# Kernel optimization log

Measured on AMD Instinct MI355X. Metric: run time of the kernel, lower is better.

Reference implementation:

```python
import jax, jax.numpy as jnp
import numpy as np
from jax import lax

B, T, D = 16, 4096, 512
L_OUT = 512          # fixed target length per batch row -> static max_label_len
THRESHOLD = 1.0
SMOOTH_FACTOR = 1.0
NOISE_THRESHOLD = 0.0


def setup_inputs() -> dict:
    key = jax.random.key(0)
    k1, k2, k3, k4 = jax.random.split(key, 4)
    hidden = jax.random.normal(k1, (B, T, D), dtype=jnp.float32)
    mask = jnp.ones((B, 1, T), dtype=jnp.float32)
    target_label_length = jnp.full((B, 1), float(L_OUT), dtype=jnp.float32)
    conv_w = jax.random.normal(k2, (D, D, 3), dtype=jnp.float32) * (1.0 / np.sqrt(3 * D))
    conv_b = jax.random.normal(k3, (D,), dtype=jnp.float32) * 0.02
    out_w = jax.random.normal(k4, (1, D), dtype=jnp.float32) * (1.0 / np.sqrt(D))
    out_b = jnp.zeros((1,), dtype=jnp.float32)
    return {"hidden": hidden, "mask": mask, "target_label_length": target_label_length,
            "conv_w": conv_w, "conv_b": conv_b, "out_w": out_w, "out_b": out_b}


def _cif(hidden, alphas, threshold, max_label_len):
    # hidden: [B,T,D], alphas: [B,T]
    b, t, d = hidden.shape

    def step(carry, xs):
        integrate, frame = carry          # [B], [B,D]
        alpha, h_t = xs                   # [B], [B,D]
        dist_completion = 1.0 - integrate
        integrate = integrate + alpha
        fires_t = integrate               # recorded BEFORE subtracting 1
        fire = integrate >= threshold
        integrate = jnp.where(fire, integrate - 1.0, integrate)
        cur = jnp.where(fire, dist_completion, alpha)
        remainds = alpha - cur
        frame = frame + cur[:, None] * h_t
        frames_t = frame                  # recorded BEFORE reset
        frame = jnp.where(fire[:, None], remainds[:, None] * h_t, frame)
        return (integrate, frame), (fires_t, frames_t)

    init = (jnp.zeros((b,), hidden.dtype), jnp.zeros((b, d), hidden.dtype))
    xs = (jnp.swapaxes(alphas, 0, 1), jnp.swapaxes(hidden, 0, 1))
    _, (fires, frames) = lax.scan(step, init, xs)
    fires = jnp.swapaxes(fires, 0, 1)     # [B,T]
    frames = jnp.swapaxes(frames, 0, 1)   # [B,T,D]

    # ragged gather of fired frames, padded to static max_label_len
    fire_mask = fires >= threshold                                  # [B,T]
    slot = jnp.cumsum(fire_mask.astype(jnp.int32), axis=1) - 1      # output slot per fire
    safe_slot = jnp.where(fire_mask, jnp.clip(slot, 0, max_label_len), max_label_len)
    out = jnp.zeros((b, max_label_len + 1, d), hidden.dtype)
    out = out.at[jnp.arange(b)[:, None], safe_slot].add(frames)     # non-fires -> dump row
    return out[:, :max_label_len, :], fires


def reference(hidden, mask, target_label_length, conv_w, conv_b, out_w, out_b):
    # conv over time: pad (l_order, r_order)=(1,1), kernel 3, relu
    x = jnp.swapaxes(hidden, 1, 2)                                  # [B,D,T]
    x = jnp.pad(x, ((0, 0), (0, 0), (1, 1)))
    y = lax.conv_general_dilated(x, conv_w, (1,), 'VALID',
                                 dimension_numbers=('NCH', 'OIH', 'NCH'))
    y = jax.nn.relu(y + conv_b[None, :, None])
    y = jnp.swapaxes(y, 1, 2)                                       # [B,T,D]
    a = y @ out_w.T + out_b                                         # [B,T,1]
    alphas = jax.nn.sigmoid(a)
    alphas = jax.nn.relu(alphas * SMOOTH_FACTOR - NOISE_THRESHOLD)
    alphas = alphas * jnp.swapaxes(mask, 1, 2)                      # [B,T,1]
    alphas = alphas[..., 0]                                         # [B,T]
    token_num = alphas.sum(-1)                                      # pre-scale sum (returned)
    target_length = target_label_length[:, 0]
    alphas = alphas * (target_length / token_num)[:, None]
    acoustic_embeds, cif_peak = _cif(hidden, alphas, THRESHOLD, L_OUT)
    return acoustic_embeds, token_num, alphas, cif_peak
```

## Files before the change

kernel.cpp:

```cpp
#include <hip/hip_runtime.h>
#include <math.h>

#define BB 16
#define TT 4096
#define DD 512
#define LOUT 512

typedef __attribute__((ext_vector_type(8))) _Float16 half8;
typedef __attribute__((ext_vector_type(4))) float floatx4;


__global__ void prep(const float* __restrict__ hidden,
                     const float* __restrict__ conv_w,
                     _Float16* __restrict__ A_hi,
                     _Float16* __restrict__ A_lo,
                     _Float16* __restrict__ B_hi,
                     _Float16* __restrict__ B_lo,
                     float* __restrict__ a_pre,
                     _Float16* __restrict__ zp) {
    int idx = blockIdx.x * 256 + threadIdx.x;
    const float4* src = (const float4*)(hidden + 8 * (size_t)idx);
    float4 v0 = src[0], v1 = src[1];
    float x[8] = {v0.x, v0.y, v0.z, v0.w, v1.x, v1.y, v1.z, v1.w};
    _Float16 hi[8], lo[8];
    #pragma unroll
    for (int j = 0; j < 8; j++) {
        hi[j] = (_Float16)x[j];
        lo[j] = (_Float16)(x[j] - (float)hi[j]);
    }
    *(half8*)(A_hi + 8 * (size_t)idx) = *(half8*)hi;
    *(half8*)(A_lo + 8 * (size_t)idx) = *(half8*)lo;

    if (idx < 786432) {
        int tap = idx / 262144;
        int rem = idx - tap * 262144;
        int c = rem >> 9;
        int i = rem & 511;
        float v = conv_w[(c * 512 + i) * 3 + tap];
        _Float16 h = (_Float16)v;
        B_hi[idx] = h;
        B_lo[idx] = (_Float16)(v - (float)h);
    }
    if (idx < 65536) a_pre[idx] = 0.f;
    if (idx < 512)   zp[idx] = (_Float16)0.f;
}

#define GLL16(g, l) __builtin_amdgcn_global_load_lds( \
    (const __attribute__((address_space(1))) void*)(g), \
    (__attribute__((address_space(3))) void*)(l), 16, 0, 0)

__launch_bounds__(256, 2)
__global__ void mfma_gemm(const char* __restrict__ wsb,
                          const float* __restrict__ conv_b,
                          const float* __restrict__ out_w,
                          float* __restrict__ a_pre) {
    __shared__ __align__(128) char lds[59392];

    const int tid  = threadIdx.x;
    const int w    = tid >> 6;
    const int lane = tid & 63;

    const int bid = blockIdx.x;
    const int swz = (bid & 7) * 256 + (bid >> 3);
    const int nt  = swz & 7;
    const int mt  = swz >> 3;
    const int b   = mt >> 4;
    const int t0  = (mt & 15) << 8;
    const int c0  = nt << 6;

    const int srow = lane >> 2;
    const int schk = lane & 3;

    int sgoff[15], sloff[15];
    #pragma unroll
    for (int j = 0; j < 15; j++) {
        const int g = w + 4 * j;
        int so = 137953344, lo = 0;
        if (g < 58) {
            if (g < 34) {
                const int dt = (g >= 17);
                const int u  = dt ? g - 17 : g;
                const int r  = 16 * u + srow;
                const int t  = t0 - 1 + r;
                const int sw = (schk ^ ((r >> 1) & 3)) << 4;
                so = (t >= 0 && t < TT) ? (dt ? 67108864 : 0)
                                          + (b * TT + t) * 1024 + sw
                                        : 137953344 + sw;
                lo = dt * 17408 + u * 1024;
            } else {
                const int h  = g - 34;
                const int dt = h / 12;
                const int rm = h % 12;
                const int tp = rm >> 2;
                const int u  = rm & 3;
                const int r  = 16 * u + srow;
                const int sw = (schk ^ ((r >> 1) & 3)) << 4;
                so = (dt ? 135790592 : 134217728) + tp * 524288
                     + (c0 + r) * 1024 + sw;
                lo = 34816 + dt * 12288 + tp * 4096 + u * 1024;
            }
        }
        sgoff[j] = so;
        sloff[j] = lo;
    }

    int aoff[12], boff[4];
    #pragma unroll
    for (int tap = 0; tap < 3; tap++)
        #pragma unroll
        for (int i = 0; i < 4; i++) {
            const int ra = 64 * w + 16 * i + (lane & 15) + tap;
            aoff[tap * 4 + i] = ra * 64
                + (((lane >> 4) ^ ((ra >> 1) & 3)) << 4);
        }
    #pragma unroll
    for (int i = 0; i < 4; i++) {
        const int rb = 16 * i + (lane & 15);
        boff[i] = rb * 64 + (((lane >> 4) ^ ((rb >> 1) & 3)) << 4);
    }

    floatx4 acc[4][4];
    #pragma unroll
    for (int mi = 0; mi < 4; mi++)
        #pragma unroll
        for (int ni = 0; ni < 4; ni++)
            acc[mi][ni] = (floatx4)(0.f);

    float u_n[4], cb_n[4];
    #pragma unroll
    for (int ni = 0; ni < 4; ni++) {
        int n = c0 + 16 * ni + (lane & 15);
        u_n[ni]  = out_w[n];
        cb_n[ni] = conv_b[n];
    }

    for (int kc = 0; kc < 16; kc++) {
        const int kb = kc << 6;

        #pragma unroll
        for (int j = 0; j < 15; j++)
            if (w + 4 * j < 58)
                GLL16(wsb + (size_t)(sgoff[j] + kb), lds + sloff[j]);
        __syncthreads();

        #pragma unroll
        for (int tap = 0; tap < 3; tap++) {
            half8 ah[4], al[4], bh[4], bl[4];
            #pragma unroll
            for (int i = 0; i < 4; i++) {
                ah[i] = *(const half8*)(lds + aoff[tap * 4 + i]);
                al[i] = *(const half8*)(lds + 17408 + aoff[tap * 4 + i]);
                bh[i] = *(const half8*)(lds + 34816 + tap * 4096 + boff[i]);
                bl[i] = *(const half8*)(lds + 47104 + tap * 4096 + boff[i]);
            }
            #pragma unroll
            for (int mi = 0; mi < 4; mi++)
                #pragma unroll
                for (int ni = 0; ni < 4; ni++)
                    acc[mi][ni] = __builtin_amdgcn_mfma_f32_16x16x32_f16(
                        ah[mi], bh[ni], acc[mi][ni], 0, 0, 0);
            #pragma unroll
            for (int mi = 0; mi < 4; mi++)
                #pragma unroll
                for (int ni = 0; ni < 4; ni++)
                    acc[mi][ni] = __builtin_amdgcn_mfma_f32_16x16x32_f16(
                        al[mi], bh[ni], acc[mi][ni], 0, 0, 0);
            #pragma unroll
            for (int mi = 0; mi < 4; mi++)
                #pragma unroll
                for (int ni = 0; ni < 4; ni++)
                    acc[mi][ni] = __builtin_amdgcn_mfma_f32_16x16x32_f16(
                        ah[mi], bl[ni], acc[mi][ni], 0, 0, 0);
        }
        __syncthreads();
    }

    float s[4][4];
    #pragma unroll
    for (int mi = 0; mi < 4; mi++)
        #pragma unroll
        for (int rg = 0; rg < 4; rg++) {
            float t = 0.f;
            #pragma unroll
            for (int ni = 0; ni < 4; ni++) {
                float y = acc[mi][ni][rg] + cb_n[ni];
                y = y > 0.f ? y : 0.f;
                t = fmaf(y, u_n[ni], t);
            }
            s[mi][rg] = t;
        }
    #pragma unroll
    for (int mi = 0; mi < 4; mi++)
        #pragma unroll
        for (int rg = 0; rg < 4; rg++) {
            #pragma unroll
            for (int off = 1; off < 16; off <<= 1)
                s[mi][rg] += __shfl_xor(s[mi][rg], off);
        }
    if ((lane & 15) == 0) {
        const int q = lane >> 4;
        #pragma unroll
        for (int mi = 0; mi < 4; mi++)
            #pragma unroll
            for (int rg = 0; rg < 4; rg++) {
                int m = 64 * w + 16 * mi + 4 * q + rg;
                atomicAdd(&a_pre[b * TT + t0 + m], s[mi][rg]);
            }
    }
}

__global__ void cif_scan(const float* __restrict__ a_pre,
                         const float* __restrict__ mask,
                         const float* __restrict__ tll,
                         const float* __restrict__ out_bias,
                         float* __restrict__ out_tn,
                         float* __restrict__ out_alphas,
                         float* __restrict__ out_peak,
                         float* __restrict__ w_main,
                         int* __restrict__ fire_pos,
                         int* __restrict__ Fcount) {
    __shared__ float alpha_s[TT];
    __shared__ float wm_s[TT];
    __shared__ float fires_s[TT];
    __shared__ int   fp_s[1024];
    __shared__ double red[256];
    __shared__ float ratio_s;
    __shared__ int   F_sh;

    const int b = blockIdx.x;
    const int tid = threadIdx.x;
    const float ob = out_bias[0];

    double lsum = 0.0;
    for (int t = tid; t < TT; t += 256) {
        float a = a_pre[b * TT + t] + ob;
        float e = expf(-fabsf(a));
        float sg = (a >= 0.f) ? (1.f / (1.f + e)) : (e / (1.f + e));
        float af = sg;
        af = af > 0.f ? af : 0.f;
        af = af * mask[b * TT + t];
        alpha_s[t] = af;
        lsum += (double)af;
    }
    red[tid] = lsum;
    __syncthreads();
    for (int off = 128; off > 0; off >>= 1) {
        if (tid < off) red[tid] += red[tid + off];
        __syncthreads();
    }
    if (tid == 0) {
        float tn = (float)red[0];
        out_tn[b] = tn;
        ratio_s = tll[b] / tn;
    }
    __syncthreads();
    const float ratio = ratio_s;

    const int t0c = tid * 16;
    float av[16];
    double csum = 0.0;
    #pragma unroll
    for (int j = 0; j < 16; j++) {
        float a = alpha_s[t0c + j] * ratio;
        av[j] = a;
        csum += (double)a;
    }
    #pragma unroll
    for (int j = 0; j < 16; j++)
        alpha_s[t0c + j] = av[j];
    red[tid] = csum;
    __syncthreads();

    #pragma unroll
    for (int off = 1; off < 256; off <<= 1) {
        double v = (tid >= off) ? red[tid - off] : 0.0;
        __syncthreads();
        red[tid] += v;
        __syncthreads();
    }
    const double base = red[tid] - csum;

    double P = base;
    int Fp = (int)P;
    #pragma unroll
    for (int j = 0; j < 16; j++) {
        const float a = av[j];
        const double Pp = P;
        P += (double)a;
        const int F = (int)P;
        fires_s[t0c + j] = (float)(P - (double)Fp);
        const bool fire = F > Fp;
        wm_s[t0c + j] = fire ? (float)((double)F - Pp) : a;
        if (fire && Fp < 1024) fp_s[Fp] = t0c + j;
        Fp = F;
    }
    if (tid == 255) {
        F_sh = (Fp > 1024) ? 1024 : Fp;
        Fcount[b] = F_sh;
    }
    __syncthreads();

    for (int t = tid; t < TT; t += 256) {
        out_alphas[b * TT + t] = alpha_s[t];
        out_peak[b * TT + t]   = fires_s[t];
        w_main[b * TT + t]     = wm_s[t];
    }
    const int F = F_sh;
    for (int s = tid; s < F; s += 256)
        fire_pos[b * 1024 + s] = fp_s[s];
}

__global__ void cif_scatter(const float* __restrict__ hidden,
                            const float* __restrict__ alphas,
                            const float* __restrict__ w_main,
                            const int* __restrict__ fire_pos,
                            const int* __restrict__ Fcount,
                            float* __restrict__ out_emb) {
    const int s = blockIdx.x;
    const int b = blockIdx.y;
    const int tid = threadIdx.x;
    const int F = Fcount[b];

    float4 acc = make_float4(0.f, 0.f, 0.f, 0.f);
    if (s < F) {
        const int t_hi = fire_pos[b * 1024 + s];
        const int t_lo = (s > 0) ? fire_pos[b * 1024 + s - 1] : 0;
        for (int t = t_lo; t <= t_hi; t++) {
            float w;
            if (s > 0 && t == t_lo)
                w = alphas[b * TT + t] - w_main[b * TT + t];
            else
                w = w_main[b * TT + t];
            const float4 h = *(const float4*)(hidden + ((size_t)(b * TT + t)) * DD + 4 * tid);
            acc.x = fmaf(w, h.x, acc.x);
            acc.y = fmaf(w, h.y, acc.y);
            acc.z = fmaf(w, h.z, acc.z);
            acc.w = fmaf(w, h.w, acc.w);
        }
    }
    *(float4*)(out_emb + ((size_t)(b * LOUT + s)) * DD + 4 * tid) = acc;
}

extern "C" void kernel_launch(void* const* d_in, const int* in_sizes, int n_in,
                              void* d_out, int out_size, void* d_ws, size_t ws_size,
                              hipStream_t stream) {
    const float* hidden  = (const float*)d_in[0];
    const float* mask    = (const float*)d_in[1];
    const float* tll     = (const float*)d_in[2];
    const float* conv_w  = (const float*)d_in[3];
    const float* conv_b  = (const float*)d_in[4];
    const float* out_w   = (const float*)d_in[5];
    const float* out_b   = (const float*)d_in[6];

    float* out        = (float*)d_out;
    float* out_emb    = out;
    float* out_tn     = out + 4194304;
    float* out_alphas = out + 4194320;
    float* out_peak   = out + 4259856;

    char* ws = (char*)d_ws;
    _Float16* A_hi   = (_Float16*)(ws);
    _Float16* A_lo   = (_Float16*)(ws + 67108864);
    _Float16* B_hi   = (_Float16*)(ws + 134217728);
    _Float16* B_lo   = (_Float16*)(ws + 135790592);
    float* a_pre     = (float*)(ws + 137363456);
    float* w_main    = (float*)(ws + 137625600);
    int*   fire_pos  = (int*)(ws + 137887744);
    int*   Fcount    = (int*)(ws + 137953280);
    _Float16* zpage  = (_Float16*)(ws + 137953344);

    prep<<<16384, 256, 0, stream>>>(hidden, conv_w, A_hi, A_lo, B_hi, B_lo,
                                    a_pre, zpage);
    mfma_gemm<<<2048, 256, 0, stream>>>(ws, conv_b, out_w, a_pre);
    cif_scan<<<16, 256, 0, stream>>>(a_pre, mask, tll, out_b,
                                     out_tn, out_alphas, out_peak,
                                     w_main, fire_pos, Fcount);
    cif_scatter<<<dim3(512, 16), 128, 0, stream>>>(hidden, out_alphas, w_main,
                                                   fire_pos, Fcount, out_emb);
}
```

Baseline: 509.9 us.

## Double-buffer LDS staging in MFMA conv GEMM to overlap loads with compute

The GEMM's K loop now uses two LDS buffers, so the async global-to-LDS loads for the next K chunk are issued while MFMAs run on the current one, with one barrier per half-step. LDS use doubles to about 116 KB through dynamic shared memory, and launch bounds drop from 2 to 1 block per CU. This trades occupancy, and with it the latency hiding that a second resident block gave, for explicit in-block overlap of memory and compute.

```diff
diff --git a/kernel.cpp b/kernel.cpp
--- a/kernel.cpp
+++ b/kernel.cpp
@@ -49,12 +49,54 @@
     (const __attribute__((address_space(1))) void*)(g), \
     (__attribute__((address_space(3))) void*)(l), 16, 0, 0)
 
-__launch_bounds__(256, 2)
+
+#define STAGE(KBX, WROFF)                                                    \
+  do {                                                                       \
+    _Pragma("unroll")                                                        \
+    for (int j_ = 0; j_ < 15; j_++)                                          \
+      if (w + 4 * j_ < 58)                                                   \
+        GLL16(wsb + (size_t)(sgoff[j_] + (KBX)), lds + (WROFF) + sloff[j_]); \
+  } while (0)
+
+#define COMPUTE(KB, RD)                                                      \
+  do {                                                                       \
+    _Pragma("unroll")                                                        \
+    for (int tap = 0; tap < 3; tap++) {                                      \
+      half8 ah[4], al[4], bh[4], bl[4];                                      \
+      _Pragma("unroll")                                                      \
+      for (int i = 0; i < 4; i++) {                                          \
+        ah[i] = *(const half8*)(lds + (RD) + aoff[tap * 4 + i]);             \
+        al[i] = *(const half8*)(lds + (RD) + 17408 + aoff[tap * 4 + i]);     \
+        bh[i] = *(const half8*)(lds + (RD) + 34816 + tap * 4096 + boff[i]);  \
+        bl[i] = *(const half8*)(lds + (RD) + 47104 + tap * 4096 + boff[i]);  \
+      }                                                                      \
+      _Pragma("unroll")                                                      \
+      for (int mi = 0; mi < 4; mi++)                                         \
+        _Pragma("unroll")                                                    \
+        for (int ni = 0; ni < 4; ni++)                                       \
+          acc[mi][ni] = __builtin_amdgcn_mfma_f32_16x16x32_f16(              \
+              ah[mi], bh[ni], acc[mi][ni], 0, 0, 0);                         \
+      _Pragma("unroll")                                                      \
+      for (int mi = 0; mi < 4; mi++)                                         \
+        _Pragma("unroll")                                                    \
+        for (int ni = 0; ni < 4; ni++)                                       \
+          acc[mi][ni] = __builtin_amdgcn_mfma_f32_16x16x32_f16(              \
+              al[mi], bh[ni], acc[mi][ni], 0, 0, 0);                         \
+      _Pragma("unroll")                                                      \
+      for (int mi = 0; mi < 4; mi++)                                         \
+        _Pragma("unroll")                                                    \
+        for (int ni = 0; ni < 4; ni++)                                       \
+          acc[mi][ni] = __builtin_amdgcn_mfma_f32_16x16x32_f16(              \
+              ah[mi], bl[ni], acc[mi][ni], 0, 0, 0);                         \
+    }                                                                        \
+  } while (0)
+
+__launch_bounds__(256, 1)
 __global__ void mfma_gemm(const char* __restrict__ wsb,
                           const float* __restrict__ conv_b,
                           const float* __restrict__ out_w,
                           float* __restrict__ a_pre) {
-    __shared__ __align__(128) char lds[59392];
+    extern __shared__ __align__(128) char lds[];
 
     const int tid  = threadIdx.x;
     const int w    = tid >> 6;
@@ -134,44 +176,16 @@
         cb_n[ni] = conv_b[n];
     }
 
-    for (int kc = 0; kc < 16; kc++) {
-        const int kb = kc << 6;
-
-        #pragma unroll
-        for (int j = 0; j < 15; j++)
-            if (w + 4 * j < 58)
-                GLL16(wsb + (size_t)(sgoff[j] + kb), lds + sloff[j]);
+    STAGE(0, 0);
+    __syncthreads();
+
+    for (int kp = 0; kp < 8; kp++) {
+        const int KB = kp << 7;
+        STAGE(KB + 64, 59392);
+        COMPUTE(KB, 0);
         __syncthreads();
-
-        #pragma unroll
-        for (int tap = 0; tap < 3; tap++) {
-            half8 ah[4], al[4], bh[4], bl[4];
-            #pragma unroll
-            for (int i = 0; i < 4; i++) {
-                ah[i] = *(const half8*)(lds + aoff[tap * 4 + i]);
-                al[i] = *(const half8*)(lds + 17408 + aoff[tap * 4 + i]);
-                bh[i] = *(const half8*)(lds + 34816 + tap * 4096 + boff[i]);
-                bl[i] = *(const half8*)(lds + 47104 + tap * 4096 + boff[i]);
-            }
-            #pragma unroll
-            for (int mi = 0; mi < 4; mi++)
-                #pragma unroll
-                for (int ni = 0; ni < 4; ni++)
-                    acc[mi][ni] = __builtin_amdgcn_mfma_f32_16x16x32_f16(
-                        ah[mi], bh[ni], acc[mi][ni], 0, 0, 0);
-            #pragma unroll
-            for (int mi = 0; mi < 4; mi++)
-                #pragma unroll
-                for (int ni = 0; ni < 4; ni++)
-                    acc[mi][ni] = __builtin_amdgcn_mfma_f32_16x16x32_f16(
-                        al[mi], bh[ni], acc[mi][ni], 0, 0, 0);
-            #pragma unroll
-            for (int mi = 0; mi < 4; mi++)
-                #pragma unroll
-                for (int ni = 0; ni < 4; ni++)
-                    acc[mi][ni] = __builtin_amdgcn_mfma_f32_16x16x32_f16(
-                        ah[mi], bl[ni], acc[mi][ni], 0, 0, 0);
-        }
+        if (kp < 7) STAGE(KB + 128, 0);
+        COMPUTE(KB + 64, 59392);
         __syncthreads();
     }
 
@@ -369,9 +383,16 @@
     int*   Fcount    = (int*)(ws + 137953280);
     _Float16* zpage  = (_Float16*)(ws + 137953344);
 
+    static bool attr_set = false;
+    if (!attr_set) {
+        hipFuncSetAttribute((const void*)mfma_gemm,
+                            hipFuncAttributeMaxDynamicSharedMemorySize, 118784);
+        attr_set = true;
+    }
+
     prep<<<16384, 256, 0, stream>>>(hidden, conv_w, A_hi, A_lo, B_hi, B_lo,
                                     a_pre, zpage);
-    mfma_gemm<<<2048, 256, 0, stream>>>(ws, conv_b, out_w, a_pre);
+    mfma_gemm<<<2048, 256, 118784, stream>>>(ws, conv_b, out_w, a_pre);
     cif_scan<<<16, 256, 0, stream>>>(a_pre, mask, tll, out_b,
                                      out_tn, out_alphas, out_peak,
                                      w_main, fire_pos, Fcount);
```

Result: slower. 550.7 us (+8.0%).
